# Kernel optimization log

Hardware: AMD Instinct MI355X
Metric: run time of the kernel (lower is better)

Reference implementation:

```python
import jax, jax.numpy as jnp
import numpy as np

B, S, D, N = 128, 1024, 512, 784  # batch, state_dim, image_feature_dim, spatial positions


def setup_inputs() -> dict:
    key = jax.random.key(0)
    ks = jax.random.split(key, 6)
    s = lambda fan_in: 1.0 / np.sqrt(fan_in)
    return {
        "in_state": jax.random.normal(ks[0], (B, S), jnp.float32),
        "image": jax.random.normal(ks[1], (B, D, N), jnp.float32),
        "Wq": jax.random.normal(ks[2], (D, S), jnp.float32) * s(S),
        "bq": jnp.zeros((D,), jnp.float32),
        "Wc": jax.random.normal(ks[3], (D, 2 * D), jnp.float32) * s(2 * D),
        "bc": jnp.zeros((D,), jnp.float32),
        "Wa": jax.random.normal(ks[4], (1, D), jnp.float32) * s(D),
        "ba": jnp.zeros((1,), jnp.float32),
        "Wo": jax.random.normal(ks[5], (S, D), jnp.float32) * s(D),
        "bo": jnp.zeros((S,), jnp.float32),
    }


def reference(in_state, image, Wq, bq, Wc, bc, Wa, ba, Wo, bo):
    # query: [B, D]
    query = in_state @ Wq.T + bq
    # broadcast multiply over spatial positions: [B, D, N]
    qimg = query[:, :, None] * image
    # cat along channel dim then permute -> [B, N, 2D]
    feats = jnp.concatenate([qimg, image], axis=1).transpose(0, 2, 1)
    # concat linear: [B, N, D]
    c = feats @ Wc.T + bc
    # attention logits: [B, N]
    logits = (c @ Wa.T + ba)[..., 0]
    attn = jax.nn.softmax(logits, axis=1)  # softmax over spatial dim
    # weighted sum over spatial positions: [B, D]
    pooled = jnp.einsum("bn,bdn->bd", attn, image)
    return pooled @ Wo.T + bo
```

## Files before the change

### kernel.cpp

```cpp
#include <hip/hip_runtime.h>
#include <math.h>

#define BB 128
#define SS 1024
#define DD 512
#define NN 784
#define NCH 8

__device__ __forceinline__ float wave_reduce_sum(float x) {
#pragma unroll
  for (int m = 32; m > 0; m >>= 1) x += __shfl_xor(x, m, 64);
  return x;
}
__device__ __forceinline__ float wave_reduce_max(float x) {
#pragma unroll
  for (int m = 32; m > 0; m >>= 1) x = fmaxf(x, __shfl_xor(x, m, 64));
  return x;
}

__global__ void k1_v(const float* __restrict__ Wa, const float* __restrict__ Wc,
                     float* __restrict__ v) {
  int k = blockIdx.x * 256 + threadIdx.x;
  int j0 = blockIdx.y * 32;
  float acc = 0.f;
#pragma unroll
  for (int j = 0; j < 32; ++j)
    acc += Wa[j0 + j] * Wc[(size_t)(j0 + j) * (2 * DD) + k];
  atomicAdd(&v[k], acc);
}

__global__ void k2_w(const float* __restrict__ in_state, const float* __restrict__ Wq,
                     const float* __restrict__ bq, const float* __restrict__ v,
                     float* __restrict__ w) {
  __shared__ float st[SS];
  int b = blockIdx.y;
  int t = threadIdx.x, lane = t & 63, wv = t >> 6;
  ((float4*)st)[t] = ((const float4*)(in_state + (size_t)b * SS))[t];
  __syncthreads();
  const float4* st4 = (const float4*)st;
  float4 s0 = st4[lane], s1 = st4[lane + 64], s2 = st4[lane + 128], s3 = st4[lane + 192];
  int d0 = blockIdx.x * 32 + wv * 8;
  float acc[8];
#pragma unroll
  for (int r = 0; r < 8; ++r) {
    const float4* q4 = (const float4*)(Wq + (size_t)(d0 + r) * SS);
    float4 a0 = q4[lane], a1 = q4[lane + 64], a2 = q4[lane + 128], a3 = q4[lane + 192];
    acc[r] = a0.x * s0.x + a0.y * s0.y + a0.z * s0.z + a0.w * s0.w
           + a1.x * s1.x + a1.y * s1.y + a1.z * s1.z + a1.w * s1.w
           + a2.x * s2.x + a2.y * s2.y + a2.z * s2.z + a2.w * s2.w
           + a3.x * s3.x + a3.y * s3.y + a3.z * s3.z + a3.w * s3.w;
  }
#pragma unroll
  for (int r = 0; r < 8; ++r) acc[r] = wave_reduce_sum(acc[r]);
  if (lane == 0) {
#pragma unroll
    for (int r = 0; r < 8; ++r) {
      int d = d0 + r;
      w[(size_t)b * DD + d] = (acc[r] + bq[d]) * v[d] + v[DD + d];
    }
  }
}

__global__ void k3_logit_part(const float* __restrict__ image, const float* __restrict__ w,
                              float* __restrict__ part) {
  __shared__ float red[8 * NN];
  int b = blockIdx.y, c = blockIdx.x;
  int t = threadIdx.x, lane = t & 63, wv = t >> 6;
  int d0 = c * 64 + wv * 8;
  const float* wp = w + (size_t)b * DD + d0;
  float wr[8];
#pragma unroll
  for (int r = 0; r < 8; ++r) wr[r] = wp[r];
  const float4* base = (const float4*)(image + ((size_t)b * DD + d0) * NN);
  float4 a0 = {0, 0, 0, 0}, a1 = {0, 0, 0, 0}, a2 = {0, 0, 0, 0}, a3 = {0, 0, 0, 0};
#pragma unroll
  for (int r = 0; r < 8; ++r) {
    const float4* row4 = base + r * 196;
    float4 x0 = row4[lane];
    float4 x1 = row4[lane + 64];
    float4 x2 = row4[lane + 128];
    float wd = wr[r];
    a0.x += x0.x * wd; a0.y += x0.y * wd; a0.z += x0.z * wd; a0.w += x0.w * wd;
    a1.x += x1.x * wd; a1.y += x1.y * wd; a1.z += x1.z * wd; a1.w += x1.w * wd;
    a2.x += x2.x * wd; a2.y += x2.y * wd; a2.z += x2.z * wd; a2.w += x2.w * wd;
  }
  if (lane < 4) {
#pragma unroll
    for (int r = 0; r < 8; ++r) {
      float4 x3 = base[r * 196 + 192 + lane];
      float wd = wr[r];
      a3.x += x3.x * wd; a3.y += x3.y * wd; a3.z += x3.z * wd; a3.w += x3.w * wd;
    }
  }
  float4* red4 = (float4*)(red + wv * NN);
  red4[lane] = a0;
  red4[lane + 64] = a1;
  red4[lane + 128] = a2;
  if (lane < 4) red4[192 + lane] = a3;
  __syncthreads();
  float* out = part + ((size_t)b * NCH + c) * NN;
  for (int n = t; n < NN; n += 512) {
    float s = red[n] + red[NN + n] + red[2 * NN + n] + red[3 * NN + n]
            + red[4 * NN + n] + red[5 * NN + n] + red[6 * NN + n] + red[7 * NN + n];
    out[n] = s;
  }
}

__global__ void k4_softmax(const float* __restrict__ part, float* __restrict__ attn) {
  __shared__ float l[NN];
  __shared__ float wred[4];
  int b = blockIdx.x, t = threadIdx.x, lane = t & 63, wv = t >> 6;
  const float* p = part + (size_t)b * NCH * NN;
  float mx = -1e30f;
  for (int n = t; n < NN; n += 256) {
    float s = 0.f;
#pragma unroll
    for (int c = 0; c < NCH; ++c) s += p[c * NN + n];
    l[n] = s;
    mx = fmaxf(mx, s);
  }
  mx = wave_reduce_max(mx);
  if (lane == 0) wred[wv] = mx;
  __syncthreads();
  mx = fmaxf(fmaxf(wred[0], wred[1]), fmaxf(wred[2], wred[3]));
  __syncthreads();
  float sum = 0.f;
  for (int n = t; n < NN; n += 256) {
    float e = __expf(l[n] - mx);
    l[n] = e;
    sum += e;
  }
  sum = wave_reduce_sum(sum);
  if (lane == 0) wred[wv] = sum;
  __syncthreads();
  float inv = 1.0f / (wred[0] + wred[1] + wred[2] + wred[3]);
  float* a = attn + (size_t)b * NN;
  for (int n = t; n < NN; n += 256) a[n] = l[n] * inv;
}

__global__ void k5_pooled(const float* __restrict__ image, const float* __restrict__ attn,
                          float* __restrict__ pooled) {
  __shared__ float a_s[NN];
  int b = blockIdx.y, t = threadIdx.x, lane = t & 63, wv = t >> 6;
  if (t < 196) ((float4*)a_s)[t] = ((const float4*)(attn + (size_t)b * NN))[t];
  __syncthreads();
  const float4* a4 = (const float4*)a_s;
  float4 aa0 = a4[lane], aa1 = a4[lane + 64], aa2 = a4[lane + 128];
  int d0 = blockIdx.x * 32 + wv * 4;
  const float4* base = (const float4*)(image + ((size_t)b * DD + d0) * NN);
  float acc[4];
#pragma unroll
  for (int r = 0; r < 4; ++r) {
    const float4* row4 = base + r * 196;
    float4 x0 = row4[lane];
    float4 x1 = row4[lane + 64];
    float4 x2 = row4[lane + 128];
    acc[r] = x0.x * aa0.x + x0.y * aa0.y + x0.z * aa0.z + x0.w * aa0.w
           + x1.x * aa1.x + x1.y * aa1.y + x1.z * aa1.z + x1.w * aa1.w
           + x2.x * aa2.x + x2.y * aa2.y + x2.z * aa2.z + x2.w * aa2.w;
  }
  if (lane < 4) {
    float4 aa3 = a4[192 + lane];
#pragma unroll
    for (int r = 0; r < 4; ++r) {
      float4 x3 = base[r * 196 + 192 + lane];
      acc[r] += x3.x * aa3.x + x3.y * aa3.y + x3.z * aa3.z + x3.w * aa3.w;
    }
  }
#pragma unroll
  for (int r = 0; r < 4; ++r) acc[r] = wave_reduce_sum(acc[r]);
  if (lane == 0) {
#pragma unroll
    for (int r = 0; r < 4; ++r) pooled[(size_t)b * DD + d0 + r] = acc[r];
  }
}

__global__ void k6_out(const float* __restrict__ pooled, const float* __restrict__ Wo,
                       const float* __restrict__ bo, float* __restrict__ out) {
  __shared__ float p_s[DD];
  int b = blockIdx.y, t = threadIdx.x, lane = t & 63, wv = t >> 6;
  ((float2*)p_s)[t] = ((const float2*)(pooled + (size_t)b * DD))[t];
  __syncthreads();
  const float4* p4 = (const float4*)p_s;
  float4 p0 = p4[lane], p1 = p4[lane + 64];
  int s0 = blockIdx.x * 32 + wv * 8;
  float acc[8];
#pragma unroll
  for (int r = 0; r < 8; ++r) {
    const float4* wo4 = (const float4*)(Wo + (size_t)(s0 + r) * DD);
    float4 x0 = wo4[lane], x1 = wo4[lane + 64];
    acc[r] = x0.x * p0.x + x0.y * p0.y + x0.z * p0.z + x0.w * p0.w
           + x1.x * p1.x + x1.y * p1.y + x1.z * p1.z + x1.w * p1.w;
  }
#pragma unroll
  for (int r = 0; r < 8; ++r) acc[r] = wave_reduce_sum(acc[r]);
  if (lane == 0) {
#pragma unroll
    for (int r = 0; r < 8; ++r) out[(size_t)b * SS + s0 + r] = acc[r] + bo[s0 + r];
  }
}

extern "C" void kernel_launch(void* const* d_in, const int* in_sizes, int n_in,
                              void* d_out, int out_size, void* d_ws, size_t ws_size,
                              hipStream_t stream) {
  const float* in_state = (const float*)d_in[0];
  const float* image    = (const float*)d_in[1];
  const float* Wq       = (const float*)d_in[2];
  const float* bq       = (const float*)d_in[3];
  const float* Wc       = (const float*)d_in[4];
  const float* Wa       = (const float*)d_in[6];
  const float* Wo       = (const float*)d_in[8];
  const float* bo       = (const float*)d_in[9];
  float* out = (float*)d_out;

  float* ws     = (float*)d_ws;
  float* v      = ws;
  float* w      = v + 2 * DD;
  float* part   = w + BB * DD;
  float* attn   = part + (size_t)BB * NCH * NN;
  float* pooled = attn + (size_t)BB * NN;

  hipMemsetAsync(v, 0, 2 * DD * sizeof(float), stream);
  k1_v<<<dim3(4, 16), 256, 0, stream>>>(Wa, Wc, v);
  k2_w<<<dim3(16, BB), 256, 0, stream>>>(in_state, Wq, bq, v, w);
  k3_logit_part<<<dim3(NCH, BB), 512, 0, stream>>>(image, w, part);
  k4_softmax<<<BB, 256, 0, stream>>>(part, attn);
  k5_pooled<<<dim3(16, BB), 512, 0, stream>>>(image, attn, pooled);
  k6_out<<<dim3(32, BB), 256, 0, stream>>>(pooled, Wo, bo, out);
}
```

Before: 379.8 us.

## Fuse logits, chunked softmax and pooling into one pass with split-softmax combine

Replaces the separate logit, softmax and pooling kernels with one kernel per (batch, spatial chunk). Each chunk computes its logits, local max and exp-sum, then reuses the same image slice, which is likely still in cache, to accumulate partial pooled vectors. A small combine kernel rescales the partials flash-attention style. This is meant to cut the second full image read and two launches. The cost is a serial wave reduction per channel row in the pooling loop, and the 49-lane row segments (15 of 64 lanes idle) may give poorly coalesced loads and low lane utilisation.

New measurement: 372.7 us. Within noise of the previous version (-1.9%).

```diff
diff --git a/kernel.cpp b/kernel.cpp
--- a/kernel.cpp
+++ b/kernel.cpp
@@ -5,7 +5,8 @@
 #define SS 1024
 #define DD 512
 #define NN 784
-#define NCH 8
+#define NCHK 4
+#define NC 196
 
 __device__ __forceinline__ float wave_reduce_sum(float x) {
 #pragma unroll
@@ -61,118 +62,93 @@
   }
 }
 
-__global__ void k3_logit_part(const float* __restrict__ image, const float* __restrict__ w,
-                              float* __restrict__ part) {
-  __shared__ float red[8 * NN];
+__global__ void k3_fused(const float* __restrict__ image, const float* __restrict__ w,
+                         float* __restrict__ P_part, float* __restrict__ mZ_part) {
+  __shared__ float w_lds[DD];
+  __shared__ float4 red[8][49];
+  __shared__ float4 u_lds[49];
+  __shared__ float p_s[DD];
   int b = blockIdx.y, c = blockIdx.x;
   int t = threadIdx.x, lane = t & 63, wv = t >> 6;
-  int d0 = c * 64 + wv * 8;
-  const float* wp = w + (size_t)b * DD + d0;
-  float wr[8];
-#pragma unroll
-  for (int r = 0; r < 8; ++r) wr[r] = wp[r];
-  const float4* base = (const float4*)(image + ((size_t)b * DD + d0) * NN);
-  float4 a0 = {0, 0, 0, 0}, a1 = {0, 0, 0, 0}, a2 = {0, 0, 0, 0}, a3 = {0, 0, 0, 0};
-#pragma unroll
-  for (int r = 0; r < 8; ++r) {
-    const float4* row4 = base + r * 196;
-    float4 x0 = row4[lane];
-    float4 x1 = row4[lane + 64];
-    float4 x2 = row4[lane + 128];
-    float wd = wr[r];
-    a0.x += x0.x * wd; a0.y += x0.y * wd; a0.z += x0.z * wd; a0.w += x0.w * wd;
-    a1.x += x1.x * wd; a1.y += x1.y * wd; a1.z += x1.z * wd; a1.w += x1.w * wd;
-    a2.x += x2.x * wd; a2.y += x2.y * wd; a2.z += x2.z * wd; a2.w += x2.w * wd;
-  }
-  if (lane < 4) {
-#pragma unroll
-    for (int r = 0; r < 8; ++r) {
-      float4 x3 = base[r * 196 + 192 + lane];
-      float wd = wr[r];
-      a3.x += x3.x * wd; a3.y += x3.y * wd; a3.z += x3.z * wd; a3.w += x3.w * wd;
-    }
-  }
-  float4* red4 = (float4*)(red + wv * NN);
-  red4[lane] = a0;
-  red4[lane + 64] = a1;
-  red4[lane + 128] = a2;
-  if (lane < 4) red4[192 + lane] = a3;
-  __syncthreads();
-  float* out = part + ((size_t)b * NCH + c) * NN;
-  for (int n = t; n < NN; n += 512) {
-    float s = red[n] + red[NN + n] + red[2 * NN + n] + red[3 * NN + n]
-            + red[4 * NN + n] + red[5 * NN + n] + red[6 * NN + n] + red[7 * NN + n];
-    out[n] = s;
-  }
-}
-
-__global__ void k4_softmax(const float* __restrict__ part, float* __restrict__ attn) {
-  __shared__ float l[NN];
-  __shared__ float wred[4];
-  int b = blockIdx.x, t = threadIdx.x, lane = t & 63, wv = t >> 6;
-  const float* p = part + (size_t)b * NCH * NN;
-  float mx = -1e30f;
-  for (int n = t; n < NN; n += 256) {
-    float s = 0.f;
-#pragma unroll
-    for (int c = 0; c < NCH; ++c) s += p[c * NN + n];
-    l[n] = s;
-    mx = fmaxf(mx, s);
-  }
-  mx = wave_reduce_max(mx);
-  if (lane == 0) wred[wv] = mx;
-  __syncthreads();
-  mx = fmaxf(fmaxf(wred[0], wred[1]), fmaxf(wred[2], wred[3]));
-  __syncthreads();
-  float sum = 0.f;
-  for (int n = t; n < NN; n += 256) {
-    float e = __expf(l[n] - mx);
-    l[n] = e;
-    sum += e;
-  }
-  sum = wave_reduce_sum(sum);
-  if (lane == 0) wred[wv] = sum;
-  __syncthreads();
-  float inv = 1.0f / (wred[0] + wred[1] + wred[2] + wred[3]);
-  float* a = attn + (size_t)b * NN;
-  for (int n = t; n < NN; n += 256) a[n] = l[n] * inv;
-}
-
-__global__ void k5_pooled(const float* __restrict__ image, const float* __restrict__ attn,
-                          float* __restrict__ pooled) {
-  __shared__ float a_s[NN];
-  int b = blockIdx.y, t = threadIdx.x, lane = t & 63, wv = t >> 6;
-  if (t < 196) ((float4*)a_s)[t] = ((const float4*)(attn + (size_t)b * NN))[t];
-  __syncthreads();
-  const float4* a4 = (const float4*)a_s;
-  float4 aa0 = a4[lane], aa1 = a4[lane + 64], aa2 = a4[lane + 128];
-  int d0 = blockIdx.x * 32 + wv * 4;
-  const float4* base = (const float4*)(image + ((size_t)b * DD + d0) * NN);
-  float acc[4];
-#pragma unroll
-  for (int r = 0; r < 4; ++r) {
-    const float4* row4 = base + r * 196;
-    float4 x0 = row4[lane];
-    float4 x1 = row4[lane + 64];
-    float4 x2 = row4[lane + 128];
-    acc[r] = x0.x * aa0.x + x0.y * aa0.y + x0.z * aa0.z + x0.w * aa0.w
-           + x1.x * aa1.x + x1.y * aa1.y + x1.z * aa1.z + x1.w * aa1.w
-           + x2.x * aa2.x + x2.y * aa2.y + x2.z * aa2.z + x2.w * aa2.w;
-  }
-  if (lane < 4) {
-    float4 aa3 = a4[192 + lane];
-#pragma unroll
-    for (int r = 0; r < 4; ++r) {
-      float4 x3 = base[r * 196 + 192 + lane];
-      acc[r] += x3.x * aa3.x + x3.y * aa3.y + x3.z * aa3.z + x3.w * aa3.w;
-    }
-  }
-#pragma unroll
-  for (int r = 0; r < 4; ++r) acc[r] = wave_reduce_sum(acc[r]);
-  if (lane == 0) {
-#pragma unroll
-    for (int r = 0; r < 4; ++r) pooled[(size_t)b * DD + d0 + r] = acc[r];
-  }
+  w_lds[t] = w[(size_t)b * DD + t];
+  __syncthreads();
+  const float4* img4 = (const float4*)image + (size_t)b * DD * 196;
+  int d0 = wv * 64;
+  const float4* pbase = img4 + (size_t)d0 * 196 + c * 49 + (lane < 49 ? lane : 48);
+  float4 acc = {0, 0, 0, 0};
+#pragma unroll 8
+  for (int i = 0; i < 64; ++i) {
+    float4 x = pbase[i * 196];
+    float wd = w_lds[d0 + i];
+    acc.x += wd * x.x; acc.y += wd * x.y; acc.z += wd * x.z; acc.w += wd * x.w;
+  }
+  if (lane < 49) red[wv][lane] = acc;
+  __syncthreads();
+  if (wv == 0) {
+    float4 l4 = {0, 0, 0, 0};
+    float lm = -1e30f;
+    if (lane < 49) {
+#pragma unroll
+      for (int v8 = 0; v8 < 8; ++v8) {
+        float4 r = red[v8][lane];
+        l4.x += r.x; l4.y += r.y; l4.z += r.z; l4.w += r.w;
+      }
+      lm = fmaxf(fmaxf(l4.x, l4.y), fmaxf(l4.z, l4.w));
+    }
+    float m = wave_reduce_max(lm);
+    float zs = 0.f;
+    if (lane < 49) {
+      float4 u4;
+      u4.x = __expf(l4.x - m); u4.y = __expf(l4.y - m);
+      u4.z = __expf(l4.z - m); u4.w = __expf(l4.w - m);
+      zs = u4.x + u4.y + u4.z + u4.w;
+      u_lds[lane] = u4;
+    }
+    float Z = wave_reduce_sum(zs);
+    if (lane == 0) {
+      mZ_part[((size_t)b * NCHK + c) * 2 + 0] = m;
+      mZ_part[((size_t)b * NCHK + c) * 2 + 1] = Z;
+    }
+  }
+  __syncthreads();
+  float4 u4 = {0, 0, 0, 0};
+  if (lane < 49) u4 = u_lds[lane];
+#pragma unroll 4
+  for (int i = 0; i < 64; ++i) {
+    float part = 0.f;
+    if (lane < 49) {
+      float4 x = pbase[i * 196];
+      part = u4.x * x.x + u4.y * x.y + u4.z * x.z + u4.w * x.w;
+    }
+    part = wave_reduce_sum(part);
+    if (lane == 0) p_s[d0 + i] = part;
+  }
+  P_part[((size_t)b * NCHK + c) * DD + d0 + lane] = p_s[d0 + lane];
+}
+
+__global__ void k5_combine(const float* __restrict__ P_part, const float* __restrict__ mZ_part,
+                           float* __restrict__ pooled) {
+  int b = blockIdx.x, t = threadIdx.x;
+  float mc[NCHK], Zc[NCHK];
+  float M = -1e30f;
+#pragma unroll
+  for (int c = 0; c < NCHK; ++c) {
+    mc[c] = mZ_part[((size_t)b * NCHK + c) * 2 + 0];
+    Zc[c] = mZ_part[((size_t)b * NCHK + c) * 2 + 1];
+    M = fmaxf(M, mc[c]);
+  }
+  float Z = 0.f, al[NCHK];
+#pragma unroll
+  for (int c = 0; c < NCHK; ++c) { al[c] = __expf(mc[c] - M); Z += al[c] * Zc[c]; }
+  float inv = 1.0f / Z;
+  float4 s = {0, 0, 0, 0};
+#pragma unroll
+  for (int c = 0; c < NCHK; ++c) {
+    float4 p = ((const float4*)P_part)[((size_t)b * NCHK + c) * 128 + t];
+    s.x += al[c] * p.x; s.y += al[c] * p.y; s.z += al[c] * p.z; s.w += al[c] * p.w;
+  }
+  s.x *= inv; s.y *= inv; s.z *= inv; s.w *= inv;
+  ((float4*)pooled)[(size_t)b * 128 + t] = s;
 }
 
 __global__ void k6_out(const float* __restrict__ pooled, const float* __restrict__ Wo,
@@ -213,18 +189,17 @@
   const float* bo       = (const float*)d_in[9];
   float* out = (float*)d_out;
 
-  float* ws     = (float*)d_ws;
-  float* v      = ws;
-  float* w      = v + 2 * DD;
-  float* part   = w + BB * DD;
-  float* attn   = part + (size_t)BB * NCH * NN;
-  float* pooled = attn + (size_t)BB * NN;
+  float* ws      = (float*)d_ws;
+  float* v       = ws;
+  float* w       = v + 2 * DD;
+  float* P_part  = w + BB * DD;
+  float* mZ_part = P_part + (size_t)BB * NCHK * DD;
+  float* pooled  = mZ_part + (size_t)BB * NCHK * 2;
 
   hipMemsetAsync(v, 0, 2 * DD * sizeof(float), stream);
   k1_v<<<dim3(4, 16), 256, 0, stream>>>(Wa, Wc, v);
   k2_w<<<dim3(16, BB), 256, 0, stream>>>(in_state, Wq, bq, v, w);
-  k3_logit_part<<<dim3(NCH, BB), 512, 0, stream>>>(image, w, part);
-  k4_softmax<<<BB, 256, 0, stream>>>(part, attn);
-  k5_pooled<<<dim3(16, BB), 512, 0, stream>>>(image, attn, pooled);
+  k3_fused<<<dim3(NCHK, BB), 512, 0, stream>>>(image, w, P_part, mZ_part);
+  k5_combine<<<BB, 128, 0, stream>>>(P_part, mZ_part, pooled);
   k6_out<<<dim3(32, BB), 256, 0, stream>>>(pooled, Wo, bo, out);
 }
```

## Fuse softmax into pooling, atomically accumulate logits, batch-reuse Wo in output GEMV

Applied to the files above, without the earlier changes.

The partial-logit buffer and the separate softmax kernel are removed. k3 now uses smaller blocks that atomically add per-position logits, and k5 recomputes the softmax max and normalizer per block before pooling, folding 1/Z into the result. Image rows are loaded up front into registers for more memory-level parallelism. k6 keeps Wo rows in registers and loops over 8 batches to cut repeated Wo reads. The costs are atomic contention, redundant softmax work in each k5 block, and higher register pressure.

Measured after the change: 377.5 us. About the same (-0.6%).

```diff
diff --git a/kernel.cpp b/kernel.cpp
--- a/kernel.cpp
+++ b/kernel.cpp
@@ -5,7 +5,7 @@
 #define SS 1024
 #define DD 512
 #define NN 784
-#define NCH 8
+#define NF4 196
 
 __device__ __forceinline__ float wave_reduce_sum(float x) {
 #pragma unroll
@@ -61,142 +61,142 @@
   }
 }
 
-__global__ void k3_logit_part(const float* __restrict__ image, const float* __restrict__ w,
-                              float* __restrict__ part) {
-  __shared__ float red[8 * NN];
-  int b = blockIdx.y, c = blockIdx.x;
-  int t = threadIdx.x, lane = t & 63, wv = t >> 6;
-  int d0 = c * 64 + wv * 8;
+__global__ void k3_logits(const float* __restrict__ image, const float* __restrict__ w,
+                          float* __restrict__ logits) {
+  __shared__ float4 red4[4][NF4];
+  int b = blockIdx.y, g = blockIdx.x;
+  int t = threadIdx.x, lane = t & 63, wv = t >> 6;
+  int d0 = g * 32 + wv * 8;
   const float* wp = w + (size_t)b * DD + d0;
   float wr[8];
 #pragma unroll
   for (int r = 0; r < 8; ++r) wr[r] = wp[r];
-  const float4* base = (const float4*)(image + ((size_t)b * DD + d0) * NN);
-  float4 a0 = {0, 0, 0, 0}, a1 = {0, 0, 0, 0}, a2 = {0, 0, 0, 0}, a3 = {0, 0, 0, 0};
-#pragma unroll
-  for (int r = 0; r < 8; ++r) {
-    const float4* row4 = base + r * 196;
-    float4 x0 = row4[lane];
-    float4 x1 = row4[lane + 64];
-    float4 x2 = row4[lane + 128];
+  const float4* base = (const float4*)image + ((size_t)b * DD + d0) * NF4;
+  float4 x0[8], x1[8], x2[8];
+#pragma unroll
+  for (int r = 0; r < 8; ++r) {
+    const float4* row = base + (size_t)r * NF4;
+    x0[r] = row[lane];
+    x1[r] = row[lane + 64];
+    x2[r] = row[lane + 128];
+  }
+  float4 a0 = {0,0,0,0}, a1 = {0,0,0,0}, a2 = {0,0,0,0}, a3 = {0,0,0,0};
+  if (lane < 4) {
+#pragma unroll
+    for (int r = 0; r < 8; ++r) {
+      float4 x3 = base[(size_t)r * NF4 + 192 + lane];
+      float wd = wr[r];
+      a3.x += wd * x3.x; a3.y += wd * x3.y; a3.z += wd * x3.z; a3.w += wd * x3.w;
+    }
+  }
+#pragma unroll
+  for (int r = 0; r < 8; ++r) {
     float wd = wr[r];
-    a0.x += x0.x * wd; a0.y += x0.y * wd; a0.z += x0.z * wd; a0.w += x0.w * wd;
-    a1.x += x1.x * wd; a1.y += x1.y * wd; a1.z += x1.z * wd; a1.w += x1.w * wd;
-    a2.x += x2.x * wd; a2.y += x2.y * wd; a2.z += x2.z * wd; a2.w += x2.w * wd;
-  }
+    a0.x += wd * x0[r].x; a0.y += wd * x0[r].y; a0.z += wd * x0[r].z; a0.w += wd * x0[r].w;
+    a1.x += wd * x1[r].x; a1.y += wd * x1[r].y; a1.z += wd * x1[r].z; a1.w += wd * x1[r].w;
+    a2.x += wd * x2[r].x; a2.y += wd * x2[r].y; a2.z += wd * x2[r].z; a2.w += wd * x2[r].w;
+  }
+  red4[wv][lane] = a0;
+  red4[wv][lane + 64] = a1;
+  red4[wv][lane + 128] = a2;
+  if (lane < 4) red4[wv][192 + lane] = a3;
+  __syncthreads();
+  const float* redf = (const float*)red4;
+  float* lg = logits + (size_t)b * NN;
+  for (int n = t; n < NN; n += 256) {
+    float s = redf[n] + redf[NN + n] + redf[2 * NN + n] + redf[3 * NN + n];
+    atomicAdd(&lg[n], s);
+  }
+}
+
+__global__ void k5_pooled(const float* __restrict__ image, const float* __restrict__ logits,
+                          float* __restrict__ pooled) {
+  __shared__ float att[NN];
+  __shared__ float wredm[4];
+  __shared__ float wredz[4];
+  int b = blockIdx.y, g = blockIdx.x;
+  int t = threadIdx.x, lane = t & 63, wv = t >> 6;
+  const float* lg = logits + (size_t)b * NN;
+  float l0 = lg[t], l1 = lg[t + 256], l2 = lg[t + 512];
+  float l3 = (t < NN - 768) ? lg[t + 768] : -1e30f;
+  float lm = fmaxf(fmaxf(l0, l1), fmaxf(l2, l3));
+  lm = wave_reduce_max(lm);
+  if (lane == 0) wredm[wv] = lm;
+  __syncthreads();
+  float m = fmaxf(fmaxf(wredm[0], wredm[1]), fmaxf(wredm[2], wredm[3]));
+  float u0 = __expf(l0 - m), u1 = __expf(l1 - m), u2 = __expf(l2 - m);
+  float u3 = (t < NN - 768) ? __expf(l3 - m) : 0.f;
+  att[t] = u0; att[t + 256] = u1; att[t + 512] = u2;
+  if (t < NN - 768) att[t + 768] = u3;
+  float zs = u0 + u1 + u2 + u3;
+  zs = wave_reduce_sum(zs);
+  if (lane == 0) wredz[wv] = zs;
+  __syncthreads();
+  float invZ = 1.0f / (wredz[0] + wredz[1] + wredz[2] + wredz[3]);
+  const float4* att4 = (const float4*)att;
+  float4 aa0 = att4[lane], aa1 = att4[lane + 64], aa2 = att4[lane + 128];
+  int d0 = g * 32 + wv * 8;
+  const float4* base = (const float4*)image + ((size_t)b * DD + d0) * NF4;
+  float4 x0[8], x1[8], x2[8];
+#pragma unroll
+  for (int r = 0; r < 8; ++r) {
+    const float4* row = base + (size_t)r * NF4;
+    x0[r] = row[lane];
+    x1[r] = row[lane + 64];
+    x2[r] = row[lane + 128];
+  }
+  float acc[8];
+#pragma unroll
+  for (int r = 0; r < 8; ++r)
+    acc[r] = x0[r].x * aa0.x + x0[r].y * aa0.y + x0[r].z * aa0.z + x0[r].w * aa0.w
+           + x1[r].x * aa1.x + x1[r].y * aa1.y + x1[r].z * aa1.z + x1[r].w * aa1.w
+           + x2[r].x * aa2.x + x2[r].y * aa2.y + x2[r].z * aa2.z + x2[r].w * aa2.w;
   if (lane < 4) {
+    float4 aa3 = att4[192 + lane];
 #pragma unroll
     for (int r = 0; r < 8; ++r) {
-      float4 x3 = base[r * 196 + 192 + lane];
-      float wd = wr[r];
-      a3.x += x3.x * wd; a3.y += x3.y * wd; a3.z += x3.z * wd; a3.w += x3.w * wd;
-    }
-  }
-  float4* red4 = (float4*)(red + wv * NN);
-  red4[lane] = a0;
-  red4[lane + 64] = a1;
-  red4[lane + 128] = a2;
-  if (lane < 4) red4[192 + lane] = a3;
-  __syncthreads();
-  float* out = part + ((size_t)b * NCH + c) * NN;
-  for (int n = t; n < NN; n += 512) {
-    float s = red[n] + red[NN + n] + red[2 * NN + n] + red[3 * NN + n]
-            + red[4 * NN + n] + red[5 * NN + n] + red[6 * NN + n] + red[7 * NN + n];
-    out[n] = s;
-  }
-}
-
-__global__ void k4_softmax(const float* __restrict__ part, float* __restrict__ attn) {
-  __shared__ float l[NN];
-  __shared__ float wred[4];
-  int b = blockIdx.x, t = threadIdx.x, lane = t & 63, wv = t >> 6;
-  const float* p = part + (size_t)b * NCH * NN;
-  float mx = -1e30f;
-  for (int n = t; n < NN; n += 256) {
-    float s = 0.f;
-#pragma unroll
-    for (int c = 0; c < NCH; ++c) s += p[c * NN + n];
-    l[n] = s;
-    mx = fmaxf(mx, s);
-  }
-  mx = wave_reduce_max(mx);
-  if (lane == 0) wred[wv] = mx;
-  __syncthreads();
-  mx = fmaxf(fmaxf(wred[0], wred[1]), fmaxf(wred[2], wred[3]));
-  __syncthreads();
-  float sum = 0.f;
-  for (int n = t; n < NN; n += 256) {
-    float e = __expf(l[n] - mx);
-    l[n] = e;
-    sum += e;
-  }
-  sum = wave_reduce_sum(sum);
-  if (lane == 0) wred[wv] = sum;
-  __syncthreads();
-  float inv = 1.0f / (wred[0] + wred[1] + wred[2] + wred[3]);
-  float* a = attn + (size_t)b * NN;
-  for (int n = t; n < NN; n += 256) a[n] = l[n] * inv;
-}
-
-__global__ void k5_pooled(const float* __restrict__ image, const float* __restrict__ attn,
-                          float* __restrict__ pooled) {
-  __shared__ float a_s[NN];
-  int b = blockIdx.y, t = threadIdx.x, lane = t & 63, wv = t >> 6;
-  if (t < 196) ((float4*)a_s)[t] = ((const float4*)(attn + (size_t)b * NN))[t];
-  __syncthreads();
-  const float4* a4 = (const float4*)a_s;
-  float4 aa0 = a4[lane], aa1 = a4[lane + 64], aa2 = a4[lane + 128];
-  int d0 = blockIdx.x * 32 + wv * 4;
-  const float4* base = (const float4*)(image + ((size_t)b * DD + d0) * NN);
-  float acc[4];
-#pragma unroll
-  for (int r = 0; r < 4; ++r) {
-    const float4* row4 = base + r * 196;
-    float4 x0 = row4[lane];
-    float4 x1 = row4[lane + 64];
-    float4 x2 = row4[lane + 128];
-    acc[r] = x0.x * aa0.x + x0.y * aa0.y + x0.z * aa0.z + x0.w * aa0.w
-           + x1.x * aa1.x + x1.y * aa1.y + x1.z * aa1.z + x1.w * aa1.w
-           + x2.x * aa2.x + x2.y * aa2.y + x2.z * aa2.z + x2.w * aa2.w;
-  }
-  if (lane < 4) {
-    float4 aa3 = a4[192 + lane];
-#pragma unroll
-    for (int r = 0; r < 4; ++r) {
-      float4 x3 = base[r * 196 + 192 + lane];
+      float4 x3 = base[(size_t)r * NF4 + 192 + lane];
       acc[r] += x3.x * aa3.x + x3.y * aa3.y + x3.z * aa3.z + x3.w * aa3.w;
     }
   }
 #pragma unroll
-  for (int r = 0; r < 4; ++r) acc[r] = wave_reduce_sum(acc[r]);
+  for (int r = 0; r < 8; ++r) acc[r] = wave_reduce_sum(acc[r]);
   if (lane == 0) {
 #pragma unroll
-    for (int r = 0; r < 4; ++r) pooled[(size_t)b * DD + d0 + r] = acc[r];
+    for (int r = 0; r < 8; ++r) pooled[(size_t)b * DD + d0 + r] = acc[r] * invZ;
   }
 }
 
 __global__ void k6_out(const float* __restrict__ pooled, const float* __restrict__ Wo,
                        const float* __restrict__ bo, float* __restrict__ out) {
-  __shared__ float p_s[DD];
-  int b = blockIdx.y, t = threadIdx.x, lane = t & 63, wv = t >> 6;
-  ((float2*)p_s)[t] = ((const float2*)(pooled + (size_t)b * DD))[t];
-  __syncthreads();
-  const float4* p4 = (const float4*)p_s;
-  float4 p0 = p4[lane], p1 = p4[lane + 64];
-  int s0 = blockIdx.x * 32 + wv * 8;
-  float acc[8];
+  int sg = blockIdx.x, bg = blockIdx.y;
+  int t = threadIdx.x, lane = t & 63, wv = t >> 6;
+  int s0 = sg * 32 + wv * 8;
+  float4 w0[8], w1[8];
 #pragma unroll
   for (int r = 0; r < 8; ++r) {
     const float4* wo4 = (const float4*)(Wo + (size_t)(s0 + r) * DD);
-    float4 x0 = wo4[lane], x1 = wo4[lane + 64];
-    acc[r] = x0.x * p0.x + x0.y * p0.y + x0.z * p0.z + x0.w * p0.w
-           + x1.x * p1.x + x1.y * p1.y + x1.z * p1.z + x1.w * p1.w;
-  }
-#pragma unroll
-  for (int r = 0; r < 8; ++r) acc[r] = wave_reduce_sum(acc[r]);
-  if (lane == 0) {
-#pragma unroll
-    for (int r = 0; r < 8; ++r) out[(size_t)b * SS + s0 + r] = acc[r] + bo[s0 + r];
+    w0[r] = wo4[lane];
+    w1[r] = wo4[lane + 64];
+  }
+  float bov[8];
+#pragma unroll
+  for (int r = 0; r < 8; ++r) bov[r] = bo[s0 + r];
+  for (int bi = 0; bi < 8; ++bi) {
+    int b = bg * 8 + bi;
+    const float4* p4 = (const float4*)(pooled + (size_t)b * DD);
+    float4 p0 = p4[lane], p1 = p4[lane + 64];
+    float acc[8];
+#pragma unroll
+    for (int r = 0; r < 8; ++r)
+      acc[r] = w0[r].x * p0.x + w0[r].y * p0.y + w0[r].z * p0.z + w0[r].w * p0.w
+             + w1[r].x * p1.x + w1[r].y * p1.y + w1[r].z * p1.z + w1[r].w * p1.w;
+#pragma unroll
+    for (int r = 0; r < 8; ++r) acc[r] = wave_reduce_sum(acc[r]);
+    if (lane == 0) {
+#pragma unroll
+      for (int r = 0; r < 8; ++r) out[(size_t)b * SS + s0 + r] = acc[r] + bov[r];
+    }
   }
 }
 
@@ -215,16 +215,14 @@
 
   float* ws     = (float*)d_ws;
   float* v      = ws;
-  float* w      = v + 2 * DD;
-  float* part   = w + BB * DD;
-  float* attn   = part + (size_t)BB * NCH * NN;
-  float* pooled = attn + (size_t)BB * NN;
-
-  hipMemsetAsync(v, 0, 2 * DD * sizeof(float), stream);
+  float* logits = v + 2 * DD;
+  float* w      = logits + (size_t)BB * NN;
+  float* pooled = w + (size_t)BB * DD;
+
+  hipMemsetAsync(ws, 0, (2 * DD + (size_t)BB * NN) * sizeof(float), stream);
   k1_v<<<dim3(4, 16), 256, 0, stream>>>(Wa, Wc, v);
   k2_w<<<dim3(16, BB), 256, 0, stream>>>(in_state, Wq, bq, v, w);
-  k3_logit_part<<<dim3(NCH, BB), 512, 0, stream>>>(image, w, part);
-  k4_softmax<<<BB, 256, 0, stream>>>(part, attn);
-  k5_pooled<<<dim3(16, BB), 512, 0, stream>>>(image, attn, pooled);
-  k6_out<<<dim3(32, BB), 256, 0, stream>>>(pooled, Wo, bo, out);
-}
+  k3_logits<<<dim3(16, BB), 256, 0, stream>>>(image, w, logits);
+  k5_pooled<<<dim3(16, BB), 256, 0, stream>>>(image, logits, pooled);
+  k6_out<<<dim3(32, 16), 256, 0, stream>>>(pooled, Wo, bo, out);
+}
```
